# Kernel tuning notes

Hardware: AMD Instinct MI355X
Metric: run time of the kernel (lower is better)

## Reference

```python
import jax, jax.numpy as jnp
import numpy as np

# Each of the 16 binary logic gates, relaxed to real values, is a multilinear
# function: gate(a,b) = c0 + c1*a + c2*b + c3*a*b. Rows follow the standard
# difflogic ordering: FALSE, AND, a&~b, a, ~a&b, b, XOR, OR, NOR, XNOR,
# ~b, a|~b, ~a, ~a|b, NAND, TRUE.
GATE_COEF = jnp.array([
    [0.0,  0.0,  0.0,  0.0],   # 0:  false
    [0.0,  0.0,  0.0,  1.0],   # 1:  a AND b
    [0.0,  1.0,  0.0, -1.0],   # 2:  a AND NOT b
    [0.0,  1.0,  0.0,  0.0],   # 3:  a
    [0.0,  0.0,  1.0, -1.0],   # 4:  NOT a AND b
    [0.0,  0.0,  1.0,  0.0],   # 5:  b
    [0.0,  1.0,  1.0, -2.0],   # 6:  a XOR b
    [0.0,  1.0,  1.0, -1.0],   # 7:  a OR b
    [1.0, -1.0, -1.0,  1.0],   # 8:  NOR
    [1.0, -1.0, -1.0,  2.0],   # 9:  XNOR
    [1.0,  0.0, -1.0,  0.0],   # 10: NOT b
    [1.0,  0.0, -1.0,  1.0],   # 11: a OR NOT b
    [1.0, -1.0,  0.0,  0.0],   # 12: NOT a
    [1.0, -1.0,  0.0,  1.0],   # 13: NOT a OR b
    [1.0,  0.0,  0.0, -1.0],   # 14: NAND
    [1.0,  0.0,  0.0,  0.0],   # 15: true
], dtype=jnp.float32)

B, IN_DIM, HIDDEN, N_LAYERS, OUT_DIM, TAU = 4096, 1024, 8192, 6, 8, 10.0
NPO = HIDDEN // OUT_DIM  # neurons_per_output


def logic_layer(h, w, ia, ib):
    # h: [B, in_dim]; w: [H, 16]; ia, ib: [H] int indices into in_dim.
    # Softmax-weighted blend of 16 gates == multilinear form with blended coefs.
    p = jax.nn.softmax(w, axis=-1)          # [H, 16]
    c = p @ GATE_COEF                       # [H, 4]
    a = h[:, ia]                            # [B, H] gather
    b = h[:, ib]                            # [B, H] gather
    return c[:, 0] + c[:, 1] * a + c[:, 2] * b + c[:, 3] * (a * b)


def setup_inputs() -> dict:
    key = jax.random.key(0)
    ks = jax.random.split(key, 8)
    return {
        "x": jax.random.uniform(ks[0], (B, IN_DIM), dtype=jnp.float32),
        "logic_w": jax.random.normal(ks[1], (N_LAYERS, HIDDEN, 16), dtype=jnp.float32),
        "scaler_w": jax.random.normal(ks[2], (OUT_DIM, OUT_DIM), dtype=jnp.float32) * 0.1,
        "scaler_b": jax.random.normal(ks[3], (OUT_DIM,), dtype=jnp.float32) * 0.1,
        "idx0_a": jax.random.randint(ks[4], (HIDDEN,), 0, IN_DIM, dtype=jnp.int32),
        "idx0_b": jax.random.randint(ks[5], (HIDDEN,), 0, IN_DIM, dtype=jnp.int32),
        "idx_a": jax.random.randint(ks[6], (N_LAYERS - 1, HIDDEN), 0, HIDDEN, dtype=jnp.int32),
        "idx_b": jax.random.randint(ks[7], (N_LAYERS - 1, HIDDEN), 0, HIDDEN, dtype=jnp.int32),
    }


def reference(x, logic_w, scaler_w, scaler_b, idx0_a, idx0_b, idx_a, idx_b):
    h = (x.reshape(x.shape[0], -1) > 0.5).astype(jnp.float32)   # binarize
    h = logic_layer(h, logic_w[0], idx0_a, idx0_b)               # [B, HIDDEN]
    for i in range(N_LAYERS - 1):
        h = logic_layer(h, logic_w[i + 1], idx_a[i], idx_b[i])
    h = h.reshape(h.shape[0], OUT_DIM, NPO)                      # [B, O, NPO]
    values = jnp.sum(h, axis=2) / TAU                            # [B, O]
    q_values = values @ scaler_w.T + scaler_b                    # nn.Linear
    return q_values
```

## Files before the change

kernel.cpp:

```cpp
#include <hip/hip_runtime.h>
#include <hip/hip_fp16.h>

constexpr int BATCH    = 4096;
constexpr int IN_DIM   = 1024;
constexpr int HIDDEN   = 8192;
constexpr int N_LAYERS = 6;
constexpr int OUT_DIM  = 8;
constexpr float INV_TAU = 0.1f;

constexpr int TB   = 4;
constexpr int NTH  = 1024;
constexpr int NPT  = HIDDEN / NTH;
constexpr int NWAVES = NTH / 64;

__device__ __forceinline__ __half2 u2h(unsigned int u) {
    union { unsigned int u; __half2 h; } v; v.u = u; return v.h;
}
__device__ __forceinline__ unsigned int h2u(__half2 h) {
    union { unsigned int u; __half2 h; } v; v.h = h; return v.u;
}

__device__ __forceinline__ uint2 pack4(float4 v) {
    __half2 lo = __float22half2_rn(make_float2(v.x, v.y));
    __half2 hi = __float22half2_rn(make_float2(v.z, v.w));
    uint2 r; r.x = h2u(lo); r.y = h2u(hi); return r;
}
__device__ __forceinline__ float4 unpack4(uint2 p) {
    float2 a = __half22float2(u2h(p.x));
    float2 b = __half22float2(u2h(p.y));
    return make_float4(a.x, a.y, b.x, b.y);
}

__global__ void prep_kernel(const float* __restrict__ logic_w,
                            const int* __restrict__ idx0_a,
                            const int* __restrict__ idx0_b,
                            const int* __restrict__ idx_a,
                            const int* __restrict__ idx_b,
                            uint2* __restrict__ coefp,
                            unsigned int* __restrict__ idxp, int n)
{
    int id = blockIdx.x * blockDim.x + threadIdx.x;
    if (id >= n) return;
    const int l = id / HIDDEN;
    const int j = id - l * HIDDEN;

    int ia, ib;
    if (l == 0) { ia = idx0_a[j]; ib = idx0_b[j]; }
    else        { ia = idx_a[(size_t)(l - 1) * HIDDEN + j];
                  ib = idx_b[(size_t)(l - 1) * HIDDEN + j]; }
    idxp[id] = (unsigned int)ia | ((unsigned int)ib << 16);

    const float4* w4 = (const float4*)(logic_w + (size_t)id * 16);
    float4 wa = w4[0], wb = w4[1], wc = w4[2], wd = w4[3];
    float wv[16] = {wa.x, wa.y, wa.z, wa.w, wb.x, wb.y, wb.z, wb.w,
                    wc.x, wc.y, wc.z, wc.w, wd.x, wd.y, wd.z, wd.w};
    float m = wv[0];
#pragma unroll
    for (int i = 1; i < 16; ++i) m = fmaxf(m, wv[i]);
    float e[16];
    float s = 0.f;
#pragma unroll
    for (int i = 0; i < 16; ++i) { e[i] = expf(wv[i] - m); s += e[i]; }
    float inv = 1.f / s;
    const float G0[16] = {0,0,0,0,0,0,0,0, 1,1,1,1,1,1,1,1};
    const float G1[16] = {0,0,1,1,0,0,1,1, -1,-1,0,0,-1,-1,0,0};
    const float G2[16] = {0,0,0,0,1,1,1,1, -1,-1,-1,-1,0,0,0,0};
    const float G3[16] = {0,1,-1,0,-1,0,-2,-1, 1,2,0,1,0,1,-1,0};
    float c0 = 0.f, c1 = 0.f, c2 = 0.f, c3 = 0.f;
#pragma unroll
    for (int i = 0; i < 16; ++i) {
        float p = e[i] * inv;
        c0 = fmaf(p, G0[i], c0);
        c1 = fmaf(p, G1[i], c1);
        c2 = fmaf(p, G2[i], c2);
        c3 = fmaf(p, G3[i], c3);
    }
    coefp[id] = pack4(make_float4(c0, c1, c2, c3));
}

__device__ __forceinline__ uint2 gateh(uint2 a, uint2 b, uint2 c) {
    __half2 cp01 = u2h(c.x), cp23 = u2h(c.y);
    __half2 c0 = __low2half2(cp01), c1 = __high2half2(cp01);
    __half2 c2 = __low2half2(cp23), c3 = __high2half2(cp23);
    __half2 alo = u2h(a.x), ahi = u2h(a.y);
    __half2 blo = u2h(b.x), bhi = u2h(b.y);
    __half2 rlo = __hfma2(blo, __hfma2(c3, alo, c2), __hfma2(c1, alo, c0));
    __half2 rhi = __hfma2(bhi, __hfma2(c3, ahi, c2), __hfma2(c1, ahi, c0));
    uint2 r; r.x = h2u(rlo); r.y = h2u(rhi); return r;
}

__global__ __launch_bounds__(NTH) void net_kernel(
    const float*  __restrict__ x,
    const uint2*  __restrict__ coefp,
    const unsigned int* __restrict__ idxp,
    const float*  __restrict__ scaler_w, const float* __restrict__ scaler_b,
    float* __restrict__ out)
{
    __shared__ uint2 h[HIDDEN];
    __shared__ uint2 hx[IN_DIM];
    __shared__ float4 warr[NWAVES];
    __shared__ float  vals[TB][OUT_DIM];

    const int tid = threadIdx.x;
    const int b0  = blockIdx.x * TB;

    {
        float4 xv;
        xv.x = (x[(size_t)(b0 + 0) * IN_DIM + tid] > 0.5f) ? 1.f : 0.f;
        xv.y = (x[(size_t)(b0 + 1) * IN_DIM + tid] > 0.5f) ? 1.f : 0.f;
        xv.z = (x[(size_t)(b0 + 2) * IN_DIM + tid] > 0.5f) ? 1.f : 0.f;
        xv.w = (x[(size_t)(b0 + 3) * IN_DIM + tid] > 0.5f) ? 1.f : 0.f;
        hx[tid] = pack4(xv);
    }
    __syncthreads();

    uint2 acc[NPT];

#pragma unroll
    for (int k = 0; k < NPT; ++k) {
        int j = k * NTH + tid;
        unsigned int pr = idxp[j];
        acc[k] = gateh(hx[pr & 0xffffu], hx[pr >> 16], coefp[j]);
    }
#pragma unroll
    for (int k = 0; k < NPT; ++k) h[k * NTH + tid] = acc[k];
    __syncthreads();

    for (int l = 1; l < N_LAYERS; ++l) {
        const unsigned int* ip = idxp  + (size_t)l * HIDDEN;
        const uint2*        cp = coefp + (size_t)l * HIDDEN;
#pragma unroll
        for (int k = 0; k < NPT; ++k) {
            int j = k * NTH + tid;
            unsigned int pr = ip[j];
            acc[k] = gateh(h[pr & 0xffffu], h[pr >> 16], cp[j]);
        }
        __syncthreads();
#pragma unroll
        for (int k = 0; k < NPT; ++k) h[k * NTH + tid] = acc[k];
        __syncthreads();
    }

    {
        const int k    = tid >> 7;
        const int base = k * 1024 + (tid & 127);
        float4 v = make_float4(0.f, 0.f, 0.f, 0.f);
#pragma unroll
        for (int i = 0; i < 8; ++i) {
            float4 t = unpack4(h[base + 128 * i]);
            v.x += t.x; v.y += t.y; v.z += t.z; v.w += t.w;
        }
#pragma unroll
        for (int off = 32; off > 0; off >>= 1) {
            v.x += __shfl_down(v.x, off);
            v.y += __shfl_down(v.y, off);
            v.z += __shfl_down(v.z, off);
            v.w += __shfl_down(v.w, off);
        }
        if ((tid & 63) == 0) warr[tid >> 6] = v;
    }
    __syncthreads();
    if (tid < OUT_DIM) {
        float4 a = warr[2 * tid], b = warr[2 * tid + 1];
        vals[0][tid] = (a.x + b.x) * INV_TAU;
        vals[1][tid] = (a.y + b.y) * INV_TAU;
        vals[2][tid] = (a.z + b.z) * INV_TAU;
        vals[3][tid] = (a.w + b.w) * INV_TAU;
    }
    __syncthreads();
    if (tid < TB * OUT_DIM) {
        int t  = tid >> 3;
        int oo = tid & 7;
        float q = scaler_b[oo];
#pragma unroll
        for (int o2 = 0; o2 < OUT_DIM; ++o2)
            q = fmaf(vals[t][o2], scaler_w[oo * OUT_DIM + o2], q);
        out[(size_t)(b0 + t) * OUT_DIM + oo] = q;
    }
}

extern "C" void kernel_launch(void* const* d_in, const int* in_sizes, int n_in,
                              void* d_out, int out_size, void* d_ws, size_t ws_size,
                              hipStream_t stream)
{
    const float* x        = (const float*)d_in[0];
    const float* logic_w  = (const float*)d_in[1];
    const float* scaler_w = (const float*)d_in[2];
    const float* scaler_b = (const float*)d_in[3];
    const int*   idx0_a   = (const int*)d_in[4];
    const int*   idx0_b   = (const int*)d_in[5];
    const int*   idx_a    = (const int*)d_in[6];
    const int*   idx_b    = (const int*)d_in[7];
    float* out = (float*)d_out;

    const int n = N_LAYERS * HIDDEN;
    uint2*        coefp = (uint2*)d_ws;
    unsigned int* idxp  = (unsigned int*)((char*)d_ws + (size_t)n * sizeof(uint2));

    prep_kernel<<<(n + 255) / 256, 256, 0, stream>>>(logic_w, idx0_a, idx0_b,
                                                     idx_a, idx_b, coefp, idxp, n);
    net_kernel<<<BATCH / TB, NTH, 0, stream>>>(x, coefp, idxp,
                                               scaler_w, scaler_b, out);
}
```

Before: 128.9 us.

## Split shared activations into two 32-bit planes and prefetch next-layer indices

Stores the packed half2 activations as two separate 32-bit shared arrays (structure of arrays) instead of one 64-bit uint2 array, so random gathers become 32-bit LDS accesses that may hit fewer bank conflicts. It also loads the next layer's index words into registers one layer ahead so their global latency overlaps the current layer's gathers. The cost is twice as many LDS gather instructions and extra registers for the prefetched indices, which could reduce occupancy.

```diff
diff --git a/kernel.cpp b/kernel.cpp
--- a/kernel.cpp
+++ b/kernel.cpp
@@ -24,11 +24,6 @@
     __half2 lo = __float22half2_rn(make_float2(v.x, v.y));
     __half2 hi = __float22half2_rn(make_float2(v.z, v.w));
     uint2 r; r.x = h2u(lo); r.y = h2u(hi); return r;
-}
-__device__ __forceinline__ float4 unpack4(uint2 p) {
-    float2 a = __half22float2(u2h(p.x));
-    float2 b = __half22float2(u2h(p.y));
-    return make_float4(a.x, a.y, b.x, b.y);
 }
 
 __global__ void prep_kernel(const float* __restrict__ logic_w,
@@ -96,8 +91,10 @@
     const float*  __restrict__ scaler_w, const float* __restrict__ scaler_b,
     float* __restrict__ out)
 {
-    __shared__ uint2 h[HIDDEN];
-    __shared__ uint2 hx[IN_DIM];
+    __shared__ unsigned int hA[HIDDEN];
+    __shared__ unsigned int hB[HIDDEN];
+    __shared__ unsigned int hxA[IN_DIM];
+    __shared__ unsigned int hxB[IN_DIM];
     __shared__ float4 warr[NWAVES];
     __shared__ float  vals[TB][OUT_DIM];
 
@@ -105,39 +102,60 @@
     const int b0  = blockIdx.x * TB;
 
     {
-        float4 xv;
-        xv.x = (x[(size_t)(b0 + 0) * IN_DIM + tid] > 0.5f) ? 1.f : 0.f;
-        xv.y = (x[(size_t)(b0 + 1) * IN_DIM + tid] > 0.5f) ? 1.f : 0.f;
-        xv.z = (x[(size_t)(b0 + 2) * IN_DIM + tid] > 0.5f) ? 1.f : 0.f;
-        xv.w = (x[(size_t)(b0 + 3) * IN_DIM + tid] > 0.5f) ? 1.f : 0.f;
-        hx[tid] = pack4(xv);
-    }
-    __syncthreads();
+        float x0 = x[(size_t)(b0 + 0) * IN_DIM + tid];
+        float x1 = x[(size_t)(b0 + 1) * IN_DIM + tid];
+        float x2 = x[(size_t)(b0 + 2) * IN_DIM + tid];
+        float x3 = x[(size_t)(b0 + 3) * IN_DIM + tid];
+        __half2 lo = __floats2half2_rn(x0 > 0.5f ? 1.f : 0.f, x1 > 0.5f ? 1.f : 0.f);
+        __half2 hi = __floats2half2_rn(x2 > 0.5f ? 1.f : 0.f, x3 > 0.5f ? 1.f : 0.f);
+        hxA[tid] = h2u(lo);
+        hxB[tid] = h2u(hi);
+    }
 
     uint2 acc[NPT];
-
+    unsigned int ij[NPT];
+    unsigned int ijn[NPT];
+
+#pragma unroll
+    for (int k = 0; k < NPT; ++k) ij[k] = idxp[k * NTH + tid];
+
+    __syncthreads();
+
+#pragma unroll
+    for (int k = 0; k < NPT; ++k) ijn[k] = idxp[HIDDEN + k * NTH + tid];
 #pragma unroll
     for (int k = 0; k < NPT; ++k) {
-        int j = k * NTH + tid;
-        unsigned int pr = idxp[j];
-        acc[k] = gateh(hx[pr & 0xffffu], hx[pr >> 16], coefp[j]);
-    }
-#pragma unroll
-    for (int k = 0; k < NPT; ++k) h[k * NTH + tid] = acc[k];
-    __syncthreads();
-
+        unsigned int pr = ij[k];
+        unsigned int ia = pr & 0xffffu, ib = pr >> 16;
+        uint2 a = make_uint2(hxA[ia], hxB[ia]);
+        uint2 b = make_uint2(hxA[ib], hxB[ib]);
+        acc[k] = gateh(a, b, coefp[k * NTH + tid]);
+    }
+#pragma unroll
+    for (int k = 0; k < NPT; ++k) { hA[k * NTH + tid] = acc[k].x; hB[k * NTH + tid] = acc[k].y; }
+    __syncthreads();
+
+#pragma unroll
     for (int l = 1; l < N_LAYERS; ++l) {
-        const unsigned int* ip = idxp  + (size_t)l * HIDDEN;
-        const uint2*        cp = coefp + (size_t)l * HIDDEN;
+#pragma unroll
+        for (int k = 0; k < NPT; ++k) ij[k] = ijn[k];
+        if (l < N_LAYERS - 1) {
+#pragma unroll
+            for (int k = 0; k < NPT; ++k)
+                ijn[k] = idxp[(size_t)(l + 1) * HIDDEN + k * NTH + tid];
+        }
+        const uint2* cp = coefp + (size_t)l * HIDDEN;
 #pragma unroll
         for (int k = 0; k < NPT; ++k) {
-            int j = k * NTH + tid;
-            unsigned int pr = ip[j];
-            acc[k] = gateh(h[pr & 0xffffu], h[pr >> 16], cp[j]);
+            unsigned int pr = ij[k];
+            unsigned int ia = pr & 0xffffu, ib = pr >> 16;
+            uint2 a = make_uint2(hA[ia], hB[ia]);
+            uint2 b = make_uint2(hA[ib], hB[ib]);
+            acc[k] = gateh(a, b, cp[k * NTH + tid]);
         }
         __syncthreads();
 #pragma unroll
-        for (int k = 0; k < NPT; ++k) h[k * NTH + tid] = acc[k];
+        for (int k = 0; k < NPT; ++k) { hA[k * NTH + tid] = acc[k].x; hB[k * NTH + tid] = acc[k].y; }
         __syncthreads();
     }
 
@@ -147,8 +165,9 @@
         float4 v = make_float4(0.f, 0.f, 0.f, 0.f);
 #pragma unroll
         for (int i = 0; i < 8; ++i) {
-            float4 t = unpack4(h[base + 128 * i]);
-            v.x += t.x; v.y += t.y; v.z += t.z; v.w += t.w;
+            float2 lo = __half22float2(u2h(hA[base + 128 * i]));
+            float2 hi = __half22float2(u2h(hB[base + 128 * i]));
+            v.x += lo.x; v.y += lo.y; v.z += hi.x; v.w += hi.y;
         }
 #pragma unroll
         for (int off = 32; off > 0; off >>= 1) {
```

Measured after the change: 131.6 us. 1.02x slower.

## Process eight batch rows per block and prefetch next layer's indices and coefficients

Applied to the files above, without the earlier changes.

Each block now handles eight batch rows packed as four half2 values per neuron (uint4), so every gathered index and coefficient is reused across twice as many samples and the grid is halved. Indices and coefficients for the next layer are loaded into registers while the current layer computes, hiding global-memory latency behind LDS gathers. Shared memory grows to 144 KB of uint4 state and register pressure rises from the prefetch buffers. The single 1024-thread block per CU may limit latency hiding.

```diff
diff --git a/kernel.cpp b/kernel.cpp
--- a/kernel.cpp
+++ b/kernel.cpp
@@ -8,7 +8,7 @@
 constexpr int OUT_DIM  = 8;
 constexpr float INV_TAU = 0.1f;
 
-constexpr int TB   = 4;
+constexpr int TB   = 8;
 constexpr int NTH  = 1024;
 constexpr int NPT  = HIDDEN / NTH;
 constexpr int NWAVES = NTH / 64;
@@ -24,11 +24,6 @@
     __half2 lo = __float22half2_rn(make_float2(v.x, v.y));
     __half2 hi = __float22half2_rn(make_float2(v.z, v.w));
     uint2 r; r.x = h2u(lo); r.y = h2u(hi); return r;
-}
-__device__ __forceinline__ float4 unpack4(uint2 p) {
-    float2 a = __half22float2(u2h(p.x));
-    float2 b = __half22float2(u2h(p.y));
-    return make_float4(a.x, a.y, b.x, b.y);
 }
 
 __global__ void prep_kernel(const float* __restrict__ logic_w,
@@ -78,15 +73,28 @@
     coefp[id] = pack4(make_float4(c0, c1, c2, c3));
 }
 
-__device__ __forceinline__ uint2 gateh(uint2 a, uint2 b, uint2 c) {
+__device__ __forceinline__ uint4 gate8(uint4 a, uint4 b, uint2 c) {
     __half2 cp01 = u2h(c.x), cp23 = u2h(c.y);
     __half2 c0 = __low2half2(cp01), c1 = __high2half2(cp01);
     __half2 c2 = __low2half2(cp23), c3 = __high2half2(cp23);
-    __half2 alo = u2h(a.x), ahi = u2h(a.y);
-    __half2 blo = u2h(b.x), bhi = u2h(b.y);
-    __half2 rlo = __hfma2(blo, __hfma2(c3, alo, c2), __hfma2(c1, alo, c0));
-    __half2 rhi = __hfma2(bhi, __hfma2(c3, ahi, c2), __hfma2(c1, ahi, c0));
-    uint2 r; r.x = h2u(rlo); r.y = h2u(rhi); return r;
+    uint4 r;
+    {
+        __half2 av = u2h(a.x), bv = u2h(b.x);
+        r.x = h2u(__hfma2(bv, __hfma2(c3, av, c2), __hfma2(c1, av, c0)));
+    }
+    {
+        __half2 av = u2h(a.y), bv = u2h(b.y);
+        r.y = h2u(__hfma2(bv, __hfma2(c3, av, c2), __hfma2(c1, av, c0)));
+    }
+    {
+        __half2 av = u2h(a.z), bv = u2h(b.z);
+        r.z = h2u(__hfma2(bv, __hfma2(c3, av, c2), __hfma2(c1, av, c0)));
+    }
+    {
+        __half2 av = u2h(a.w), bv = u2h(b.w);
+        r.w = h2u(__hfma2(bv, __hfma2(c3, av, c2), __hfma2(c1, av, c0)));
+    }
+    return r;
 }
 
 __global__ __launch_bounds__(NTH) void net_kernel(
@@ -96,44 +104,64 @@
     const float*  __restrict__ scaler_w, const float* __restrict__ scaler_b,
     float* __restrict__ out)
 {
-    __shared__ uint2 h[HIDDEN];
-    __shared__ uint2 hx[IN_DIM];
-    __shared__ float4 warr[NWAVES];
-    __shared__ float  vals[TB][OUT_DIM];
+    __shared__ uint4 h[HIDDEN];
+    __shared__ uint4 hx[IN_DIM];
+    __shared__ float warr[NWAVES][TB];
+    __shared__ float vals[TB][OUT_DIM];
 
     const int tid = threadIdx.x;
     const int b0  = blockIdx.x * TB;
 
     {
-        float4 xv;
-        xv.x = (x[(size_t)(b0 + 0) * IN_DIM + tid] > 0.5f) ? 1.f : 0.f;
-        xv.y = (x[(size_t)(b0 + 1) * IN_DIM + tid] > 0.5f) ? 1.f : 0.f;
-        xv.z = (x[(size_t)(b0 + 2) * IN_DIM + tid] > 0.5f) ? 1.f : 0.f;
-        xv.w = (x[(size_t)(b0 + 3) * IN_DIM + tid] > 0.5f) ? 1.f : 0.f;
-        hx[tid] = pack4(xv);
-    }
-    __syncthreads();
-
-    uint2 acc[NPT];
+        float v[TB];
+#pragma unroll
+        for (int r = 0; r < TB; ++r)
+            v[r] = (x[(size_t)(b0 + r) * IN_DIM + tid] > 0.5f) ? 1.f : 0.f;
+        uint4 p;
+        p.x = h2u(__floats2half2_rn(v[0], v[1]));
+        p.y = h2u(__floats2half2_rn(v[2], v[3]));
+        p.z = h2u(__floats2half2_rn(v[4], v[5]));
+        p.w = h2u(__floats2half2_rn(v[6], v[7]));
+        hx[tid] = p;
+    }
+
+    uint4 acc[NPT];
+    unsigned int ij[NPT], ijn[NPT];
+    uint2 cf[NPT], cfn[NPT];
+
+#pragma unroll
+    for (int k = 0; k < NPT; ++k) { ij[k] = idxp[k * NTH + tid]; cf[k] = coefp[k * NTH + tid]; }
+
+    __syncthreads();
 
 #pragma unroll
     for (int k = 0; k < NPT; ++k) {
-        int j = k * NTH + tid;
-        unsigned int pr = idxp[j];
-        acc[k] = gateh(hx[pr & 0xffffu], hx[pr >> 16], coefp[j]);
+        ijn[k] = idxp[HIDDEN + k * NTH + tid];
+        cfn[k] = coefp[HIDDEN + k * NTH + tid];
+    }
+#pragma unroll
+    for (int k = 0; k < NPT; ++k) {
+        unsigned int pr = ij[k];
+        acc[k] = gate8(hx[pr & 0xffffu], hx[pr >> 16], cf[k]);
     }
 #pragma unroll
     for (int k = 0; k < NPT; ++k) h[k * NTH + tid] = acc[k];
     __syncthreads();
 
     for (int l = 1; l < N_LAYERS; ++l) {
-        const unsigned int* ip = idxp  + (size_t)l * HIDDEN;
-        const uint2*        cp = coefp + (size_t)l * HIDDEN;
+#pragma unroll
+        for (int k = 0; k < NPT; ++k) { ij[k] = ijn[k]; cf[k] = cfn[k]; }
+        if (l < N_LAYERS - 1) {
+#pragma unroll
+            for (int k = 0; k < NPT; ++k) {
+                ijn[k] = idxp[(size_t)(l + 1) * HIDDEN + k * NTH + tid];
+                cfn[k] = coefp[(size_t)(l + 1) * HIDDEN + k * NTH + tid];
+            }
+        }
 #pragma unroll
         for (int k = 0; k < NPT; ++k) {
-            int j = k * NTH + tid;
-            unsigned int pr = ip[j];
-            acc[k] = gateh(h[pr & 0xffffu], h[pr >> 16], cp[j]);
+            unsigned int pr = ij[k];
+            acc[k] = gate8(h[pr & 0xffffu], h[pr >> 16], cf[k]);
         }
         __syncthreads();
 #pragma unroll
@@ -144,38 +172,42 @@
     {
         const int k    = tid >> 7;
         const int base = k * 1024 + (tid & 127);
-        float4 v = make_float4(0.f, 0.f, 0.f, 0.f);
+        float s[TB] = {0.f, 0.f, 0.f, 0.f, 0.f, 0.f, 0.f, 0.f};
 #pragma unroll
         for (int i = 0; i < 8; ++i) {
-            float4 t = unpack4(h[base + 128 * i]);
-            v.x += t.x; v.y += t.y; v.z += t.z; v.w += t.w;
+            uint4 t = h[base + 128 * i];
+            float2 f0 = __half22float2(u2h(t.x));
+            float2 f1 = __half22float2(u2h(t.y));
+            float2 f2 = __half22float2(u2h(t.z));
+            float2 f3 = __half22float2(u2h(t.w));
+            s[0] += f0.x; s[1] += f0.y; s[2] += f1.x; s[3] += f1.y;
+            s[4] += f2.x; s[5] += f2.y; s[6] += f3.x; s[7] += f3.y;
         }
 #pragma unroll
         for (int off = 32; off > 0; off >>= 1) {
-            v.x += __shfl_down(v.x, off);
-            v.y += __shfl_down(v.y, off);
-            v.z += __shfl_down(v.z, off);
-            v.w += __shfl_down(v.w, off);
-        }
-        if ((tid & 63) == 0) warr[tid >> 6] = v;
-    }
-    __syncthreads();
-    if (tid < OUT_DIM) {
-        float4 a = warr[2 * tid], b = warr[2 * tid + 1];
-        vals[0][tid] = (a.x + b.x) * INV_TAU;
-        vals[1][tid] = (a.y + b.y) * INV_TAU;
-        vals[2][tid] = (a.z + b.z) * INV_TAU;
-        vals[3][tid] = (a.w + b.w) * INV_TAU;
+#pragma unroll
+            for (int r = 0; r < TB; ++r) s[r] += __shfl_down(s[r], off);
+        }
+        if ((tid & 63) == 0) {
+#pragma unroll
+            for (int r = 0; r < TB; ++r) warr[tid >> 6][r] = s[r];
+        }
     }
     __syncthreads();
     if (tid < TB * OUT_DIM) {
-        int t  = tid >> 3;
-        int oo = tid & 7;
-        float q = scaler_b[oo];
-#pragma unroll
-        for (int o2 = 0; o2 < OUT_DIM; ++o2)
-            q = fmaf(vals[t][o2], scaler_w[oo * OUT_DIM + o2], q);
-        out[(size_t)(b0 + t) * OUT_DIM + oo] = q;
+        int r = tid >> 3;
+        int k = tid & 7;
+        vals[r][k] = (warr[2 * k][r] + warr[2 * k + 1][r]) * INV_TAU;
+    }
+    __syncthreads();
+    if (tid < TB * OUT_DIM) {
+        int r = tid >> 3;
+        int o = tid & 7;
+        float q = scaler_b[o];
+#pragma unroll
+        for (int k = 0; k < OUT_DIM; ++k)
+            q = fmaf(vals[r][k], scaler_w[o * OUT_DIM + k], q);
+        out[(size_t)(b0 + r) * OUT_DIM + o] = q;
     }
 }
 
```

After: 117.5 us. 1.1x faster.
